# Optimization experiments

Measured on AMD Instinct MI355X. Metric: run time of the kernel, lower is better.

## Reference

```python
import jax, jax.numpy as jnp
import numpy as np

N_NODES = 100000
N_EDGES = 1600000
D_IN, D_HID, D_OUT = 64, 64, 40


def glorot(key, fan_in, fan_out):
    lim = np.sqrt(6.0 / (fan_in + fan_out))
    return jax.random.uniform(key, (fan_in, fan_out), jnp.float32, -lim, lim)


def setup_inputs() -> dict:
    key = jax.random.key(0)
    ks = jax.random.split(key, 8)
    x = jax.random.normal(ks[0], (N_NODES, D_IN), dtype=jnp.float32)
    edge_index = jax.random.randint(ks[1], (2, N_EDGES), 0, N_NODES, dtype=jnp.int32)
    return {
        "x": x,
        "edge_index": edge_index,
        "W1": glorot(ks[2], D_IN, D_HID),
        "b1": jnp.zeros((D_HID,), jnp.float32),
        "W2": glorot(ks[3], D_HID, D_HID),
        "b2": jnp.zeros((D_HID,), jnp.float32),
        "W3": glorot(ks[4], D_HID, D_OUT),
        "b3": jnp.zeros((D_OUT,), jnp.float32),
    }


def gcn_conv(x, src, dst, W, b):
    """PyG GCNConv: x@W, symmetric norm with self-loops, scatter-add, +bias.
    src/dst already include self-loops."""
    n = x.shape[0]
    ew = jnp.ones(src.shape[0], dtype=x.dtype)
    deg = jax.ops.segment_sum(ew, dst, num_segments=n)  # in-degree incl. self-loop
    dis = jnp.where(deg > 0, jax.lax.rsqrt(deg), 0.0)
    norm = dis[src] * dis[dst]                          # [E+N]
    h = x @ W                                           # [N, d_out]
    msg = h[src] * norm[:, None]                        # gather + scale
    out = jax.ops.segment_sum(msg, dst, num_segments=n) # scatter-add at dst
    return out + b


def reference(x, edge_index, W1, b1, W2, b2, W3, b3):
    n = x.shape[0]
    loop = jnp.arange(n, dtype=edge_index.dtype)
    src = jnp.concatenate([edge_index[0], loop])
    dst = jnp.concatenate([edge_index[1], loop])
    h = jax.nn.relu(gcn_conv(x, src, dst, W1, b1))
    h = jax.nn.relu(gcn_conv(h, src, dst, W2, b2))
    h = gcn_conv(h, src, dst, W3, b3)
    return jax.nn.log_softmax(h, axis=-1)
```

## Files before the change

### kernel.cpp

```cpp
#include <hip/hip_runtime.h>
#include <hip/hip_fp16.h>
#include <math.h>


static inline size_t align256(size_t x) { return (x + 255) & ~(size_t)255; }

#define NBLK 512
#define BTHR 1024
#define MAXB 6144

using f16x8 = __attribute__((ext_vector_type(8))) _Float16;
using f32x4 = __attribute__((ext_vector_type(4))) float;
union U16 { uint4 u; f16x8 h; };

__device__ __forceinline__ __half2 u2h(unsigned u) { union { unsigned u; __half2 h; } t; t.u = u; return t.h; }
__device__ __forceinline__ unsigned h2u(__half2 h) { union { unsigned u; __half2 h; } t; t.h = h; return t.u; }

template<int NW>
__device__ __forceinline__ int block_excl_scan(int v, int t, int* wsum) {
    int lane = t & 63, w = t >> 6;
    int incl = v;
    #pragma unroll
    for (int off = 1; off < 64; off <<= 1) {
        int u = __shfl_up(incl, off, 64);
        if (lane >= off) incl += u;
    }
    if (lane == 63) wsum[w] = incl;
    __syncthreads();
    if (t == 0) {
        int acc = 0;
        #pragma unroll
        for (int i = 0; i < NW; ++i) { int x = wsum[i]; wsum[i] = acc; acc += x; }
    }
    __syncthreads();
    return incl - v + wsum[w];
}

__global__ void k_zero(const float* __restrict__ W1, const float* __restrict__ W2,
                       const float* __restrict__ W3, uint4* __restrict__ Wh1,
                       uint4* __restrict__ Wh2, uint4* __restrict__ Wh3,
                       int* __restrict__ bucketCnt, int* __restrict__ degHist, int nb) {
    int b = blockIdx.x;
    int t = threadIdx.x;
    if (b == 3) {
        for (int i = t; i < nb * 16; i += 512) bucketCnt[i] = 0;
        if (t < 64) degHist[t] = 0;
        return;
    }
    const float* W = (b == 0) ? W1 : (b == 1) ? W2 : W3;
    uint4* Wh = (b == 0) ? Wh1 : (b == 1) ? Wh2 : Wh3;
    int dout = (b == 2) ? 40 : 64, ntc = (b == 2) ? 3 : 4;
    int total = 2 * ntc * 64;
    if (t < total) {
        int l = t & 63, nt = (t >> 6) % ntc, kh = t / (ntc * 64);
        int g = l >> 4, j = l & 15;
        int n = nt * 16 + j;
        float v[8];
        #pragma unroll
        for (int ee = 0; ee < 8; ++ee) {
            int k = kh * 32 + g * 8 + ee;
            v[ee] = (n < dout) ? W[k * dout + n] : 0.f;
        }
        uint4 o;
        o.x = h2u(__floats2half2_rn(v[0], v[1]));
        o.y = h2u(__floats2half2_rn(v[2], v[3]));
        o.z = h2u(__floats2half2_rn(v[4], v[5]));
        o.w = h2u(__floats2half2_rn(v[6], v[7]));
        Wh[t] = o;
    }
}

__global__ __launch_bounds__(BTHR) void k_bucket2(const int* __restrict__ src,
                                                  const int* __restrict__ dst,
                                                  int* __restrict__ bucketCnt,
                                                  int* __restrict__ sorted,
                                                  int e, int nb, int chunk) {
    __shared__ int h[512];
    __shared__ int cur[512];
    int t = threadIdx.x;
    for (int i = t; i < nb; i += BTHR) h[i] = 0;
    __syncthreads();
    int b0 = blockIdx.x * chunk, b1 = min(b0 + chunk, e);
    for (int i = b0 + t; i < b1; i += BTHR)
        atomicAdd(&h[dst[i] >> 8], 1);
    __syncthreads();
    for (int i = t; i < nb; i += BTHR) {
        int cnt = h[i];
        cur[i] = cnt ? atomicAdd(&bucketCnt[i * 16], cnt) : 0;
    }
    __syncthreads();
    for (int i = b0 + t; i < b1; i += BTHR) {
        int d = dst[i];
        int b = d >> 8;
        int pos = atomicAdd(&cur[b], 1);
        if (pos < MAXB)
            sorted[b * MAXB + pos] = src[i] | ((d & 255) << 17);
    }
}

__global__ void k_csr2(const int* __restrict__ bucketCnt, const int* __restrict__ sorted,
                       int* __restrict__ eidx, int2* __restrict__ rowdeg,
                       float* __restrict__ dis, int* __restrict__ degHist, int n) {
    __shared__ int pk[MAXB];
    __shared__ int pk2[MAXB];
    __shared__ int deg[256];
    __shared__ int cur[256];
    __shared__ int wsum[4];
    __shared__ int dh[64];
    int k = blockIdx.x;
    int base = k * MAXB;
    int m = min(bucketCnt[k * 16], MAXB);
    int t = threadIdx.x;
    deg[t] = 0;
    if (t < 64) dh[t] = 0;
    __syncthreads();
    for (int j = t; j < m; j += 256) {
        int v = sorted[base + j];
        pk[j] = v;
        atomicAdd(&deg[(v >> 17) & 255], 1);
    }
    __syncthreads();
    int dv = deg[t];
    int excl = block_excl_scan<4>(dv, t, wsum);
    int node = (k << 8) + t;
    if (node < n) {
        rowdeg[node] = make_int2(base + excl, dv);
        dis[node] = rsqrtf((float)(dv + 1));
        atomicAdd(&dh[min(dv, 63)], 1);
    }
    cur[t] = excl;
    __syncthreads();
    if (t < 64 && dh[t]) atomicAdd(&degHist[t], dh[t]);
    for (int j = t; j < m; j += 256) {
        int v = pk[j];
        int pos = atomicAdd(&cur[(v >> 17) & 255], 1);
        pk2[pos] = v & 0x1FFFF;
    }
    __syncthreads();
    for (int j = t; j < m; j += 256)
        eidx[base + j] = pk2[j];
}

__global__ void k_dscan(const int* __restrict__ degHist, int* __restrict__ cursor) {
    int t = threadIdx.x;
    int v = degHist[t];
    int incl = v;
    #pragma unroll
    for (int off = 1; off < 64; off <<= 1) {
        int u = __shfl_up(incl, off, 64);
        if (t >= off) incl += u;
    }
    cursor[t] = incl - v;
}

__global__ void k_dorder(const int2* __restrict__ rowdeg, int* __restrict__ cursor,
                         int* __restrict__ perm, int n) {
    __shared__ int lh[64], lbase[64];
    int t = threadIdx.x;
    int i = blockIdx.x * 256 + t;
    if (t < 64) lh[t] = 0;
    __syncthreads();
    int bin = 0, lrank = 0;
    bool vld = i < n;
    if (vld) {
        bin = min(rowdeg[i].y, 63);
        lrank = atomicAdd(&lh[bin], 1);
    }
    __syncthreads();
    if (t < 64 && lh[t]) lbase[t] = atomicAdd(&cursor[t], lh[t]);
    __syncthreads();
    if (vld) perm[lbase[bin] + lrank] = i;
}

template<int DOUT, int NT>
__global__ __launch_bounds__(256) void k_mfgemm(const float* __restrict__ Xv,
                                                const uint4* __restrict__ Wh,
                                                const float* __restrict__ dis,
                                                uint4* __restrict__ HS2, int n) {
    constexpr int STR = NT * 16 + 8;
    __shared__ __align__(16) _Float16 tile[4][16][STR];
    int wid = threadIdx.x >> 6, l = threadIdx.x & 63;
    int row0 = (blockIdx.x * 4 + wid) * 16;
    int g = l >> 4, j = l & 15;
    int rowA = min(row0 + j, n - 1);

    U16 bf[2][NT];
    #pragma unroll
    for (int kh = 0; kh < 2; ++kh)
        #pragma unroll
        for (int nt = 0; nt < NT; ++nt)
            bf[kh][nt].u = Wh[(kh * NT + nt) * 64 + l];

    U16 a0, a1;
    const float4* xr = (const float4*)Xv + (size_t)rowA * 16;
    float4 f0 = xr[g * 2], f1 = xr[g * 2 + 1];
    float4 f2 = xr[8 + g * 2], f3 = xr[8 + g * 2 + 1];
    a0.u.x = h2u(__floats2half2_rn(f0.x, f0.y)); a0.u.y = h2u(__floats2half2_rn(f0.z, f0.w));
    a0.u.z = h2u(__floats2half2_rn(f1.x, f1.y)); a0.u.w = h2u(__floats2half2_rn(f1.z, f1.w));
    a1.u.x = h2u(__floats2half2_rn(f2.x, f2.y)); a1.u.y = h2u(__floats2half2_rn(f2.z, f2.w));
    a1.u.z = h2u(__floats2half2_rn(f3.x, f3.y)); a1.u.w = h2u(__floats2half2_rn(f3.z, f3.w));

    f32x4 acc[NT];
    #pragma unroll
    for (int nt = 0; nt < NT; ++nt) acc[nt] = (f32x4){0.f, 0.f, 0.f, 0.f};
    #pragma unroll
    for (int nt = 0; nt < NT; ++nt) {
        acc[nt] = __builtin_amdgcn_mfma_f32_16x16x32_f16(a0.h, bf[0][nt].h, acc[nt], 0, 0, 0);
        acc[nt] = __builtin_amdgcn_mfma_f32_16x16x32_f16(a1.h, bf[1][nt].h, acc[nt], 0, 0, 0);
    }

    float4 d4 = *(const float4*)(dis + row0 + g * 4);
    float dd[4] = {d4.x, d4.y, d4.z, d4.w};
    #pragma unroll
    for (int nt = 0; nt < NT; ++nt)
        #pragma unroll
        for (int r = 0; r < 4; ++r)
            tile[wid][g * 4 + r][nt * 16 + j] = (_Float16)(acc[nt][r] * dd[r]);
    __builtin_amdgcn_wave_barrier();
    constexpr int C8 = DOUT / 8;
    #pragma unroll
    for (int idx = 0; idx < (16 * C8 + 63) / 64; ++idx) {
        int ii = idx * 64 + l;
        if (ii < 16 * C8) {
            int rr = ii / C8, c = ii % C8;
            if (row0 + rr < n) {
                uint4 v = *(const uint4*)((const char*)&tile[wid][rr][0] + c * 16);
                HS2[(size_t)(row0 + rr) * C8 + c] = v;
            }
        }
    }
}

template<int DOUT, int NT>
__global__ __launch_bounds__(256) void k_fgg(const int2* __restrict__ rowdeg,
                                             const int* __restrict__ eidx,
                                             const int* __restrict__ perm,
                                             const uint4* __restrict__ tbl,
                                             const float* __restrict__ dis,
                                             const float* __restrict__ bias,
                                             const uint4* __restrict__ Wh,
                                             uint4* __restrict__ outTbl, int n) {
    __shared__ __align__(16) uint4 At[16][9];
    constexpr int CSTR = NT * 16 + 8;
    __shared__ __align__(16) _Float16 Ct[16][CSTR];
    __shared__ int   smNode[16];
    __shared__ float smDis[16];
    int tid = threadIdx.x, wid = tid >> 6, lane = tid & 63;
    int nn = lane >> 4, q = (lane >> 3) & 1, c = lane & 7;
    int j16 = wid * 4 + nn;
    int pos = blockIdx.x * 16 + j16;
    bool vld = pos < n;
    int node = vld ? perm[pos] : 0;
    int2 rd = rowdeg[node];
    int s0 = rd.x;
    int d = vld ? rd.y : 0;
    float ds = dis[node];
    const float4* bp = (const float4*)(bias + 8 * c);
    float4 bA = bp[0], bB = bp[1];
    __half2 a0 = u2h(0u), a1 = u2h(0u), a2 = u2h(0u), a3 = u2h(0u);
    if (q == 0 && vld) {
        uint4 v = tbl[(unsigned)node * 8 + c];
        a0 = u2h(v.x); a1 = u2h(v.y); a2 = u2h(v.z); a3 = u2h(v.w);
    }
    const int* ep = eidx + s0;
    int k = 0;
    for (; k + 8 <= d; k += 8) {
        int e0 = ep[k + q], e1 = ep[k + 2 + q], e2 = ep[k + 4 + q], e3 = ep[k + 6 + q];
        uint4 v0 = tbl[(unsigned)e0 * 8 + c];
        uint4 v1 = tbl[(unsigned)e1 * 8 + c];
        uint4 v2 = tbl[(unsigned)e2 * 8 + c];
        uint4 v3 = tbl[(unsigned)e3 * 8 + c];
        a0 = __hadd2(a0, u2h(v0.x)); a1 = __hadd2(a1, u2h(v0.y));
        a2 = __hadd2(a2, u2h(v0.z)); a3 = __hadd2(a3, u2h(v0.w));
        a0 = __hadd2(a0, u2h(v1.x)); a1 = __hadd2(a1, u2h(v1.y));
        a2 = __hadd2(a2, u2h(v1.z)); a3 = __hadd2(a3, u2h(v1.w));
        a0 = __hadd2(a0, u2h(v2.x)); a1 = __hadd2(a1, u2h(v2.y));
        a2 = __hadd2(a2, u2h(v2.z)); a3 = __hadd2(a3, u2h(v2.w));
        a0 = __hadd2(a0, u2h(v3.x)); a1 = __hadd2(a1, u2h(v3.y));
        a2 = __hadd2(a2, u2h(v3.z)); a3 = __hadd2(a3, u2h(v3.w));
    }
    for (; k + 4 <= d; k += 4) {
        int e0 = ep[k + q], e1 = ep[k + 2 + q];
        uint4 v0 = tbl[(unsigned)e0 * 8 + c];
        uint4 v1 = tbl[(unsigned)e1 * 8 + c];
        a0 = __hadd2(a0, u2h(v0.x)); a1 = __hadd2(a1, u2h(v0.y));
        a2 = __hadd2(a2, u2h(v0.z)); a3 = __hadd2(a3, u2h(v0.w));
        a0 = __hadd2(a0, u2h(v1.x)); a1 = __hadd2(a1, u2h(v1.y));
        a2 = __hadd2(a2, u2h(v1.z)); a3 = __hadd2(a3, u2h(v1.w));
    }
    {
        int i0 = k + q, i1 = k + 2 + q;
        if (i0 < d) {
            uint4 v = tbl[(unsigned)ep[i0] * 8 + c];
            a0 = __hadd2(a0, u2h(v.x)); a1 = __hadd2(a1, u2h(v.y));
            a2 = __hadd2(a2, u2h(v.z)); a3 = __hadd2(a3, u2h(v.w));
        }
        if (i1 < d) {
            uint4 v = tbl[(unsigned)ep[i1] * 8 + c];
            a0 = __hadd2(a0, u2h(v.x)); a1 = __hadd2(a1, u2h(v.y));
            a2 = __hadd2(a2, u2h(v.z)); a3 = __hadd2(a3, u2h(v.w));
        }
    }
    unsigned w0 = h2u(a0), w1 = h2u(a1), w2 = h2u(a2), w3 = h2u(a3);
    w0 = h2u(__hadd2(u2h(w0), u2h((unsigned)__shfl_xor((int)w0, 8, 64))));
    w1 = h2u(__hadd2(u2h(w1), u2h((unsigned)__shfl_xor((int)w1, 8, 64))));
    w2 = h2u(__hadd2(u2h(w2), u2h((unsigned)__shfl_xor((int)w2, 8, 64))));
    w3 = h2u(__hadd2(u2h(w3), u2h((unsigned)__shfl_xor((int)w3, 8, 64))));
    if (q == 0) {
        float2 f0 = __half22float2(u2h(w0));
        float2 f1 = __half22float2(u2h(w1));
        float2 f2 = __half22float2(u2h(w2));
        float2 f3 = __half22float2(u2h(w3));
        float v0 = fmaxf(f0.x * ds + bA.x, 0.f), v1 = fmaxf(f0.y * ds + bA.y, 0.f);
        float v2 = fmaxf(f1.x * ds + bA.z, 0.f), v3 = fmaxf(f1.y * ds + bA.w, 0.f);
        float v4 = fmaxf(f2.x * ds + bB.x, 0.f), v5 = fmaxf(f2.y * ds + bB.y, 0.f);
        float v6 = fmaxf(f3.x * ds + bB.z, 0.f), v7 = fmaxf(f3.y * ds + bB.w, 0.f);
        uint4 o;
        o.x = h2u(__floats2half2_rn(v0, v1));
        o.y = h2u(__floats2half2_rn(v2, v3));
        o.z = h2u(__floats2half2_rn(v4, v5));
        o.w = h2u(__floats2half2_rn(v6, v7));
        At[j16][c] = o;
        if (c == 0) { smNode[j16] = vld ? node : -1; smDis[j16] = ds; }
    }
    __syncthreads();
    int g = lane >> 4, jj = lane & 15;
    U16 fa0, fa1;
    fa0.u = At[jj][g];
    fa1.u = At[jj][4 + g];
    f32x4 acc = (f32x4){0.f, 0.f, 0.f, 0.f};
    if (wid < NT) {
        U16 fb0, fb1;
        fb0.u = Wh[(0 * NT + wid) * 64 + lane];
        fb1.u = Wh[(1 * NT + wid) * 64 + lane];
        acc = __builtin_amdgcn_mfma_f32_16x16x32_f16(fa0.h, fb0.h, acc, 0, 0, 0);
        acc = __builtin_amdgcn_mfma_f32_16x16x32_f16(fa1.h, fb1.h, acc, 0, 0, 0);
        #pragma unroll
        for (int r = 0; r < 4; ++r)
            Ct[g * 4 + r][wid * 16 + jj] = (_Float16)(acc[r] * smDis[g * 4 + r]);
    }
    __syncthreads();
    constexpr int C8o = DOUT / 8;
    constexpr int OSTR = (DOUT == 40) ? 8 : C8o;
    if (tid < 16 * C8o) {
        int j = tid / C8o, cc = tid % C8o;
        int nd = smNode[j];
        if (nd >= 0) {
            uint4 v = *(const uint4*)((const char*)&Ct[j][0] + cc * 16);
            outTbl[(unsigned)nd * OSTR + cc] = v;
        }
    }
}

template<int DOUT>
__global__ __launch_bounds__(256) void k_gather4(const int2* __restrict__ rowdeg,
                                                 const int* __restrict__ eidx,
                                                 const int* __restrict__ perm,
                                                 const uint4* __restrict__ tbl,
                                                 const float* __restrict__ dis,
                                                 const float* __restrict__ b,
                                                 float* __restrict__ outp, int n) {
    constexpr int C8 = DOUT / 8;
    constexpr int TSTR = (DOUT == 40) ? 8 : C8;
    int wave = (blockIdx.x * blockDim.x + threadIdx.x) >> 6;
    int lane = threadIdx.x & 63;
    int nn = lane >> 4, q = (lane >> 3) & 1, c = lane & 7;
    int pos = wave * 4 + nn;
    bool vld = pos < n;
    int node = vld ? perm[pos] : 0;
    int2 rd = rowdeg[node];
    int s0 = rd.x;
    int d = vld ? rd.y : 0;
    bool act = vld && (c < C8);
    float ds = dis[node];
    float4 bA = make_float4(0.f, 0.f, 0.f, 0.f), bB = bA;
    if (act) {
        const float4* bp = (const float4*)(b + 8 * c);
        bA = bp[0]; bB = bp[1];
    }
    __half2 a0 = u2h(0u), a1 = u2h(0u), a2 = u2h(0u), a3 = u2h(0u);
    if (q == 0 && act) {
        uint4 v = tbl[(unsigned)node * TSTR + c];
        a0 = u2h(v.x); a1 = u2h(v.y); a2 = u2h(v.z); a3 = u2h(v.w);
    }
    const int* ep = eidx + s0;
    int k = 0;
    for (; k + 8 <= d; k += 8) {
        int e0 = ep[k + q], e1 = ep[k + 2 + q], e2 = ep[k + 4 + q], e3 = ep[k + 6 + q];
        if (act) {
            uint4 v0 = tbl[(unsigned)e0 * TSTR + c];
            uint4 v1 = tbl[(unsigned)e1 * TSTR + c];
            uint4 v2 = tbl[(unsigned)e2 * TSTR + c];
            uint4 v3 = tbl[(unsigned)e3 * TSTR + c];
            a0 = __hadd2(a0, u2h(v0.x)); a1 = __hadd2(a1, u2h(v0.y));
            a2 = __hadd2(a2, u2h(v0.z)); a3 = __hadd2(a3, u2h(v0.w));
            a0 = __hadd2(a0, u2h(v1.x)); a1 = __hadd2(a1, u2h(v1.y));
            a2 = __hadd2(a2, u2h(v1.z)); a3 = __hadd2(a3, u2h(v1.w));
            a0 = __hadd2(a0, u2h(v2.x)); a1 = __hadd2(a1, u2h(v2.y));
            a2 = __hadd2(a2, u2h(v2.z)); a3 = __hadd2(a3, u2h(v2.w));
            a0 = __hadd2(a0, u2h(v3.x)); a1 = __hadd2(a1, u2h(v3.y));
            a2 = __hadd2(a2, u2h(v3.z)); a3 = __hadd2(a3, u2h(v3.w));
        }
    }
    for (; k + 4 <= d; k += 4) {
        int e0 = ep[k + q], e1 = ep[k + 2 + q];
        if (act) {
            uint4 v0 = tbl[(unsigned)e0 * TSTR + c];
            uint4 v1 = tbl[(unsigned)e1 * TSTR + c];
            a0 = __hadd2(a0, u2h(v0.x)); a1 = __hadd2(a1, u2h(v0.y));
            a2 = __hadd2(a2, u2h(v0.z)); a3 = __hadd2(a3, u2h(v0.w));
            a0 = __hadd2(a0, u2h(v1.x)); a1 = __hadd2(a1, u2h(v1.y));
            a2 = __hadd2(a2, u2h(v1.z)); a3 = __hadd2(a3, u2h(v1.w));
        }
    }
    {
        int i0 = k + q, i1 = k + 2 + q;
        if (act && i0 < d) {
            uint4 v = tbl[(unsigned)ep[i0] * TSTR + c];
            a0 = __hadd2(a0, u2h(v.x)); a1 = __hadd2(a1, u2h(v.y));
            a2 = __hadd2(a2, u2h(v.z)); a3 = __hadd2(a3, u2h(v.w));
        }
        if (act && i1 < d) {
            uint4 v = tbl[(unsigned)ep[i1] * TSTR + c];
            a0 = __hadd2(a0, u2h(v.x)); a1 = __hadd2(a1, u2h(v.y));
            a2 = __hadd2(a2, u2h(v.z)); a3 = __hadd2(a3, u2h(v.w));
        }
    }
    unsigned w0 = h2u(a0), w1 = h2u(a1), w2 = h2u(a2), w3 = h2u(a3);
    w0 = h2u(__hadd2(u2h(w0), u2h((unsigned)__shfl_xor((int)w0, 8, 64))));
    w1 = h2u(__hadd2(u2h(w1), u2h((unsigned)__shfl_xor((int)w1, 8, 64))));
    w2 = h2u(__hadd2(u2h(w2), u2h((unsigned)__shfl_xor((int)w2, 8, 64))));
    w3 = h2u(__hadd2(u2h(w3), u2h((unsigned)__shfl_xor((int)w3, 8, 64))));
    float2 f0 = __half22float2(u2h(w0));
    float2 f1 = __half22float2(u2h(w1));
    float2 f2 = __half22float2(u2h(w2));
    float2 f3 = __half22float2(u2h(w3));
    float v0 = f0.x * ds + bA.x, v1 = f0.y * ds + bA.y;
    float v2 = f1.x * ds + bA.z, v3 = f1.y * ds + bA.w;
    float v4 = f2.x * ds + bB.x, v5 = f2.y * ds + bB.y;
    float v6 = f3.x * ds + bB.z, v7 = f3.y * ds + bB.w;
    float m = act ? fmaxf(fmaxf(fmaxf(v0, v1), fmaxf(v2, v3)),
                          fmaxf(fmaxf(v4, v5), fmaxf(v6, v7))) : -INFINITY;
    #pragma unroll
    for (int off = 1; off <= 4; off <<= 1) m = fmaxf(m, __shfl_xor(m, off, 64));
    float s = act ? (__expf(v0 - m) + __expf(v1 - m) + __expf(v2 - m) + __expf(v3 - m) +
                     __expf(v4 - m) + __expf(v5 - m) + __expf(v6 - m) + __expf(v7 - m)) : 0.f;
    #pragma unroll
    for (int off = 1; off <= 4; off <<= 1) s += __shfl_xor(s, off, 64);
    float ls = __logf(s);
    if (q == 0 && act) {
        float* op = outp + (size_t)node * DOUT + 8 * c;
        *(float4*)op = make_float4(v0 - m - ls, v1 - m - ls, v2 - m - ls, v3 - m - ls);
        *(float4*)(op + 4) = make_float4(v4 - m - ls, v5 - m - ls, v6 - m - ls, v7 - m - ls);
    }
}

extern "C" void kernel_launch(void* const* d_in, const int* in_sizes, int n_in,
                              void* d_out, int out_size, void* d_ws, size_t ws_size,
                              hipStream_t stream) {
    const float* x  = (const float*)d_in[0];
    const int*   ei = (const int*)d_in[1];
    const float* W1 = (const float*)d_in[2];
    const float* b1 = (const float*)d_in[3];
    const float* W2 = (const float*)d_in[4];
    const float* b2 = (const float*)d_in[5];
    const float* W3 = (const float*)d_in[6];
    const float* b3 = (const float*)d_in[7];
    float* out = (float*)d_out;

    const int N = in_sizes[0] / 64;
    const int E = in_sizes[1] / 2;
    const int* src = ei;
    const int* dst = ei + E;
    const int NB = (N + 255) >> 8;
    const int CHUNK = (E + NBLK - 1) / NBLK;

    char* ws = (char*)d_ws;
    size_t off = 0;
    int2*     rowdeg     = (int2*)(ws + off);     off = align256(off + (size_t)N * 8);
    float*    dis        = (float*)(ws + off);    off = align256(off + (size_t)N * 4);
    int*      bucketCnt  = (int*)(ws + off);      off = align256(off + (size_t)NB * 16 * 4);
    int*      degHist    = (int*)(ws + off);      off = align256(off + 64 * 4);
    int*      cursor     = (int*)(ws + off);      off = align256(off + 64 * 4);
    int*      perm       = (int*)(ws + off);      off = align256(off + (size_t)N * 4);
    uint4*    Wh1        = (uint4*)(ws + off);    off = align256(off + 512 * 16);
    uint4*    Wh2        = (uint4*)(ws + off);    off = align256(off + 512 * 16);
    uint4*    Wh3        = (uint4*)(ws + off);    off = align256(off + 384 * 16);
    int*      eidx       = (int*)(ws + off);      off = align256(off + (size_t)NB * MAXB * 4);
    uint4*    hsA        = (uint4*)(ws + off);    off = align256(off + (size_t)N * 32 * 4);
    uint4*    hsB        = (uint4*)(ws + off);    off = align256(off + (size_t)N * 32 * 4);
    int*   sorted = (int*)hsB;
    uint4* hsA40  = hsA;
    (void)ws_size; (void)n_in; (void)out_size;

    const int B = 256;
    auto cdiv = [](long a, long b) { return (int)((a + b - 1) / b); };

    k_zero<<<4, 512, 0, stream>>>(W1, W2, W3, Wh1, Wh2, Wh3, bucketCnt, degHist, NB);
    k_bucket2<<<NBLK, BTHR, 0, stream>>>(src, dst, bucketCnt, sorted, E, NB, CHUNK);
    k_csr2<<<NB, B, 0, stream>>>(bucketCnt, sorted, eidx, rowdeg, dis, degHist, N);
    k_dscan<<<1, 64, 0, stream>>>(degHist, cursor);
    k_dorder<<<NB, B, 0, stream>>>(rowdeg, cursor, perm, N);

    const int GG   = cdiv(N, 64);
    const int GFGG = cdiv(N, 16);
    const int GATH = cdiv((long)cdiv(N, 4) * 64, B);

    k_mfgemm<64, 4><<<GG, B, 0, stream>>>(x, Wh1, dis, hsA, N);
    k_fgg<64, 4><<<GFGG, B, 0, stream>>>(rowdeg, eidx, perm, hsA, dis, b1, Wh2, hsB, N);
    k_fgg<40, 3><<<GFGG, B, 0, stream>>>(rowdeg, eidx, perm, hsB, dis, b2, Wh3, hsA40, N);
    k_gather4<40><<<GATH, B, 0, stream>>>(rowdeg, eidx, perm, hsA40, dis, b3, out, N);
}
```

Before: 157.0 us.

## Fuse degree-ordering into CSR kernel with block-local perm and wider blocks

Drops the global degree histogram, its scan kernel and the separate ordering kernel. Each CSR block now sorts its own 256 nodes by degree into a local slice of perm. The CSR kernel also goes from 256 to 1024 threads per block. This removes two launches and a global atomic pass, but node ordering is now only per bucket, which may weaken load balance in the later gather kernels.

```diff
diff --git a/kernel.cpp b/kernel.cpp
--- a/kernel.cpp
+++ b/kernel.cpp
@@ -39,12 +39,11 @@
 __global__ void k_zero(const float* __restrict__ W1, const float* __restrict__ W2,
                        const float* __restrict__ W3, uint4* __restrict__ Wh1,
                        uint4* __restrict__ Wh2, uint4* __restrict__ Wh3,
-                       int* __restrict__ bucketCnt, int* __restrict__ degHist, int nb) {
+                       int* __restrict__ bucketCnt, int nb) {
     int b = blockIdx.x;
     int t = threadIdx.x;
     if (b == 3) {
         for (int i = t; i < nb * 16; i += 512) bucketCnt[i] = 0;
-        if (t < 64) degHist[t] = 0;
         return;
     }
     const float* W = (b == 0) ? W1 : (b == 1) ? W2 : W3;
@@ -98,78 +97,67 @@
     }
 }
 
-__global__ void k_csr2(const int* __restrict__ bucketCnt, const int* __restrict__ sorted,
-                       int* __restrict__ eidx, int2* __restrict__ rowdeg,
-                       float* __restrict__ dis, int* __restrict__ degHist, int n) {
+__global__ __launch_bounds__(BTHR) void k_csr2(const int* __restrict__ bucketCnt,
+                                               const int* __restrict__ sorted,
+                                               int* __restrict__ eidx,
+                                               int2* __restrict__ rowdeg,
+                                               float* __restrict__ dis,
+                                               int* __restrict__ perm, int n) {
     __shared__ int pk[MAXB];
     __shared__ int pk2[MAXB];
     __shared__ int deg[256];
     __shared__ int cur[256];
-    __shared__ int wsum[4];
-    __shared__ int dh[64];
+    __shared__ int wsum[16];
+    __shared__ int dh[64], dhBase[64];
     int k = blockIdx.x;
     int base = k * MAXB;
     int m = min(bucketCnt[k * 16], MAXB);
     int t = threadIdx.x;
-    deg[t] = 0;
+    if (t < 256) deg[t] = 0;
     if (t < 64) dh[t] = 0;
     __syncthreads();
-    for (int j = t; j < m; j += 256) {
+    for (int j = t; j < m; j += BTHR) {
         int v = sorted[base + j];
         pk[j] = v;
         atomicAdd(&deg[(v >> 17) & 255], 1);
     }
     __syncthreads();
-    int dv = deg[t];
-    int excl = block_excl_scan<4>(dv, t, wsum);
+    int dv = (t < 256) ? deg[t] : 0;
+    int excl = block_excl_scan<16>(dv, t, wsum);
     int node = (k << 8) + t;
-    if (node < n) {
+    bool isNode = (t < 256) && (node < n);
+    int bin = min(dv, 63);
+    if (isNode) {
         rowdeg[node] = make_int2(base + excl, dv);
         dis[node] = rsqrtf((float)(dv + 1));
-        atomicAdd(&dh[min(dv, 63)], 1);
-    }
-    cur[t] = excl;
-    __syncthreads();
-    if (t < 64 && dh[t]) atomicAdd(&degHist[t], dh[t]);
-    for (int j = t; j < m; j += 256) {
+        atomicAdd(&dh[bin], 1);
+    }
+    if (t < 256) cur[t] = excl;
+    __syncthreads();
+    if (t < 64) {
+        int v = dh[t];
+        int incl = v;
+        #pragma unroll
+        for (int off = 1; off < 64; off <<= 1) {
+            int u = __shfl_up(incl, off, 64);
+            if (t >= off) incl += u;
+        }
+        dhBase[t] = incl - v;
+        dh[t] = 0;
+    }
+    __syncthreads();
+    if (isNode) {
+        int lrank = atomicAdd(&dh[bin], 1);
+        perm[(k << 8) + dhBase[bin] + lrank] = node;
+    }
+    for (int j = t; j < m; j += BTHR) {
         int v = pk[j];
         int pos = atomicAdd(&cur[(v >> 17) & 255], 1);
         pk2[pos] = v & 0x1FFFF;
     }
     __syncthreads();
-    for (int j = t; j < m; j += 256)
+    for (int j = t; j < m; j += BTHR)
         eidx[base + j] = pk2[j];
-}
-
-__global__ void k_dscan(const int* __restrict__ degHist, int* __restrict__ cursor) {
-    int t = threadIdx.x;
-    int v = degHist[t];
-    int incl = v;
-    #pragma unroll
-    for (int off = 1; off < 64; off <<= 1) {
-        int u = __shfl_up(incl, off, 64);
-        if (t >= off) incl += u;
-    }
-    cursor[t] = incl - v;
-}
-
-__global__ void k_dorder(const int2* __restrict__ rowdeg, int* __restrict__ cursor,
-                         int* __restrict__ perm, int n) {
-    __shared__ int lh[64], lbase[64];
-    int t = threadIdx.x;
-    int i = blockIdx.x * 256 + t;
-    if (t < 64) lh[t] = 0;
-    __syncthreads();
-    int bin = 0, lrank = 0;
-    bool vld = i < n;
-    if (vld) {
-        bin = min(rowdeg[i].y, 63);
-        lrank = atomicAdd(&lh[bin], 1);
-    }
-    __syncthreads();
-    if (t < 64 && lh[t]) lbase[t] = atomicAdd(&cursor[t], lh[t]);
-    __syncthreads();
-    if (vld) perm[lbase[bin] + lrank] = i;
 }
 
 template<int DOUT, int NT>
@@ -480,9 +468,7 @@
     int2*     rowdeg     = (int2*)(ws + off);     off = align256(off + (size_t)N * 8);
     float*    dis        = (float*)(ws + off);    off = align256(off + (size_t)N * 4);
     int*      bucketCnt  = (int*)(ws + off);      off = align256(off + (size_t)NB * 16 * 4);
-    int*      degHist    = (int*)(ws + off);      off = align256(off + 64 * 4);
-    int*      cursor     = (int*)(ws + off);      off = align256(off + 64 * 4);
-    int*      perm       = (int*)(ws + off);      off = align256(off + (size_t)N * 4);
+    int*      perm       = (int*)(ws + off);      off = align256(off + (size_t)NB * 256 * 4);
     uint4*    Wh1        = (uint4*)(ws + off);    off = align256(off + 512 * 16);
     uint4*    Wh2        = (uint4*)(ws + off);    off = align256(off + 512 * 16);
     uint4*    Wh3        = (uint4*)(ws + off);    off = align256(off + 384 * 16);
@@ -496,11 +482,9 @@
     const int B = 256;
     auto cdiv = [](long a, long b) { return (int)((a + b - 1) / b); };
 
-    k_zero<<<4, 512, 0, stream>>>(W1, W2, W3, Wh1, Wh2, Wh3, bucketCnt, degHist, NB);
+    k_zero<<<4, 512, 0, stream>>>(W1, W2, W3, Wh1, Wh2, Wh3, bucketCnt, NB);
     k_bucket2<<<NBLK, BTHR, 0, stream>>>(src, dst, bucketCnt, sorted, E, NB, CHUNK);
-    k_csr2<<<NB, B, 0, stream>>>(bucketCnt, sorted, eidx, rowdeg, dis, degHist, N);
-    k_dscan<<<1, 64, 0, stream>>>(degHist, cursor);
-    k_dorder<<<NB, B, 0, stream>>>(rowdeg, cursor, perm, N);
+    k_csr2<<<NB, BTHR, 0, stream>>>(bucketCnt, sorted, eidx, rowdeg, dis, perm, N);
 
     const int GG   = cdiv(N, 64);
     const int GFGG = cdiv(N, 16);
```

After: 158.2 us. No clear change (+0.8%).
